# Optimization experiments

Measured on AMD Instinct MI355X. Metric: run time of the kernel, lower is better.

The kernel has to match this reference:

```python
import jax, jax.numpy as jnp
import numpy as np

C = 1.0
MIN_NORM = 1e-15
BALL_EPS = 4e-3  # hgcn eps for float32 in proj

def _norm(v):
    return jnp.maximum(jnp.linalg.norm(v, axis=-1, keepdims=True), MIN_NORM)

def artanh(y):
    return jnp.arctanh(jnp.clip(y, -1.0 + 1e-7, 1.0 - 1e-7))

def logmap0(p, c):
    sqrt_c = c ** 0.5
    pn = _norm(p)
    return p / (sqrt_c * pn) * artanh(sqrt_c * pn)

def expmap0(u, c):
    sqrt_c = c ** 0.5
    un = _norm(u)
    return jnp.tanh(sqrt_c * un) * u / (sqrt_c * un)

def proj(x, c):
    xn = _norm(x)
    maxnorm = (1.0 - BALL_EPS) / (c ** 0.5)
    return jnp.where(xn > maxnorm, x / xn * maxnorm, x)

def setup_inputs() -> dict:
    key = jax.random.key(0)
    k1, k2, k3, k4 = jax.random.split(key, 4)
    N, E, F = 100000, 640000, 128
    # points inside the Poincare ball
    x = 0.01 * jax.random.normal(k1, (N, F), dtype=jnp.float32)
    adj = jax.random.randint(k2, (2, E), 0, N, dtype=jnp.int64)
    edge_attr = jax.random.normal(k3, (E, F), dtype=jnp.float32)
    att_w = jax.random.normal(k4, (1, 3 * F), dtype=jnp.float32) * (1.0 / np.sqrt(3 * F))
    att_b = jnp.zeros((1,), dtype=jnp.float32)
    return {"x": x, "adj": adj, "edge_attr": edge_attr, "att_w": att_w, "att_b": att_b}

def reference(x, adj, edge_attr, att_w, att_b):
    N = x.shape[0]
    src, dst = adj[0], adj[1]  # agg_direction='in' -> i = 0
    xt = logmap0(x, C)  # [N, F] tangent features
    xs = xt[src]        # [E, F] gathered neighbor tangent feats
    # DenseAtt: sigmoid(Linear(cat(x_i, x_j, edge_attr)))
    feats = jnp.concatenate([xs, xt[dst], edge_attr], axis=-1)  # [E, 3F]
    adj_att = jax.nn.sigmoid(feats @ att_w.T + att_b)           # [E, 1]
    ones = jnp.ones((src.shape[0], 1), dtype=xt.dtype)
    agg_add = jax.ops.segment_sum(xs * adj_att, src, num_segments=N)
    cnt_src = jnp.maximum(jax.ops.segment_sum(ones, src, num_segments=N), 1.0)
    cnt_dst = jnp.maximum(jax.ops.segment_sum(ones, dst, num_segments=N), 1.0)
    mean_src = jax.ops.segment_sum(edge_attr, src, num_segments=N) / cnt_src
    mean_dst = jax.ops.segment_sum(edge_attr, dst, num_segments=N) / cnt_dst
    support_t = xt + agg_add + mean_src + mean_dst
    return proj(expmap0(support_t, C), C)
```

## Files before the change

### kernel.cpp

```cpp
#include <hip/hip_runtime.h>
#include <math.h>

#define F 128
#define WAVE 64
#define CAP 64
#define LSLOT 32

__global__ void k_zero(int* __restrict__ p, int n) {
    int i = blockIdx.x * blockDim.x + threadIdx.x;
    if (i < n) p[i] = 0;
}

__device__ __forceinline__ float halfwave_reduce_sum(float v) {
#pragma unroll
    for (int off = 16; off >= 1; off >>= 1)
        v += __shfl_xor(v, off, 64);
    return v;
}

__global__ void k_prenode(const float* __restrict__ x, const float* __restrict__ w,
                          float* __restrict__ a_s, float* __restrict__ a_d, int N) {
    int row = blockIdx.x * (blockDim.x >> 5) + (threadIdx.x >> 5);
    int fl = threadIdx.x & 31;
    if (row >= N) return;
    float4 v = ((const float4*)(x + (size_t)row * F))[fl];
    float ss = halfwave_reduce_sum(v.x * v.x + v.y * v.y + v.z * v.z + v.w * v.w);
    float pn = fmaxf(sqrtf(ss), 1e-15f);
    float y = fminf(pn, 1.0f - 1e-7f);
    float at = 0.5f * __logf((1.0f + y) / (1.0f - y));
    float s = at / pn;
    float4 o = make_float4(v.x * s, v.y * s, v.z * s, v.w * s);
    float4 W0 = ((const float4*)w)[fl];
    float4 W1 = ((const float4*)(w + F))[fl];
    float d0 = halfwave_reduce_sum(o.x * W0.x + o.y * W0.y + o.z * W0.z + o.w * W0.w);
    float d1 = halfwave_reduce_sum(o.x * W1.x + o.y * W1.y + o.z * W1.z + o.w * W1.w);
    if (fl == 0) { a_s[row] = d0; a_d[row] = d1; }
}

__global__ void k_fill(const int* __restrict__ src, const int* __restrict__ dst,
                       const float* __restrict__ a_d,
                       int* __restrict__ cur_src, int* __restrict__ cur_dst,
                       int* __restrict__ elist_src, int* __restrict__ elist_dst,
                       float* __restrict__ ad_e, int E) {
    int e = blockIdx.x * blockDim.x + threadIdx.x;
    if (e >= E) return;
    int s = src[e], d = dst[e];
    ad_e[e] = a_d[d];
    int ps = atomicAdd(&cur_src[s], 1);
    if (ps < CAP) elist_src[(size_t)s * CAP + ps] = e;
    int pd = atomicAdd(&cur_dst[d], 1);
    if (pd < CAP) elist_dst[(size_t)d * CAP + pd] = e;
}

__global__ __launch_bounds__(128) void
k_aggfinal(const float* __restrict__ x, const float* __restrict__ eattr,
           const int* __restrict__ cur_src, const int* __restrict__ cur_dst,
           const int* __restrict__ elist_src, const int* __restrict__ elist_dst,
           const float* __restrict__ a_s, const float* __restrict__ ad_e,
           const float* __restrict__ w, const float* __restrict__ bptr,
           float* __restrict__ out, int N) {
    __shared__ float dot_lds[2][LSLOT * 33];
    int wid  = threadIdx.x >> 6;
    int lane = threadIdx.x & (WAVE - 1);
    int n = blockIdx.x * 2 + wid;
    if (n >= N) return;
    float* dlds = dot_lds[wid];
    int half = lane >> 5;
    int fl   = lane & 31;

    int cS = cur_src[n]; int degS = cS < CAP ? cS : CAP;
    int cD = cur_dst[n]; int degD = cD < CAP ? cD : CAP;
    int e_lnS = (lane < degS) ? elist_src[(size_t)n * CAP + lane] : 0;
    int e_lnD = (lane < degD) ? elist_dst[(size_t)n * CAP + lane] : 0;
    float advl = (lane < degS) ? ad_e[e_lnS] : 0.f;

    float4 W2 = ((const float4*)(w + 2 * F))[fl];
    float a_sn = a_s[n];
    float bias = bptr[0];

    float4 accS0 = make_float4(0.f, 0.f, 0.f, 0.f), accS1 = accS0;
    float4 accD0 = accS0, accD1 = accS0;
    float attsum_fb = 0.f;
    int degM = degS > degD ? degS : degD;
    for (int i = 0; i < degM; i += 4) {
        int idx0 = i + half;
        int idx1 = i + 2 + half;
        int eS0 = __shfl(e_lnS, idx0, 64);
        int eS1 = __shfl(e_lnS, idx1, 64);
        int eD0 = __shfl(e_lnD, idx0, 64);
        int eD1 = __shfl(e_lnD, idx1, 64);
        if (idx0 < degD) {
            float4 v = ((const float4*)(eattr + (size_t)eD0 * F))[fl];
            accD0.x += v.x; accD0.y += v.y; accD0.z += v.z; accD0.w += v.w;
        }
        if (idx1 < degD) {
            float4 v = ((const float4*)(eattr + (size_t)eD1 * F))[fl];
            accD1.x += v.x; accD1.y += v.y; accD1.z += v.z; accD1.w += v.w;
        }
        if (idx0 < degS) {
            float4 v = ((const float4*)(eattr + (size_t)eS0 * F))[fl];
            accS0.x += v.x; accS0.y += v.y; accS0.z += v.z; accS0.w += v.w;
            float p = v.x * W2.x + v.y * W2.y + v.z * W2.z + v.w * W2.w;
            if (idx0 < LSLOT) {
                dlds[idx0 * 33 + fl] = p;
            } else {
                float adv = __shfl(advl, idx0, 64);
                float dotv = halfwave_reduce_sum(p);
                attsum_fb += 1.0f / (1.0f + __expf(-(a_sn + adv + dotv + bias)));
            }
        }
        if (idx1 < degS) {
            float4 v = ((const float4*)(eattr + (size_t)eS1 * F))[fl];
            accS1.x += v.x; accS1.y += v.y; accS1.z += v.z; accS1.w += v.w;
            float p = v.x * W2.x + v.y * W2.y + v.z * W2.z + v.w * W2.w;
            if (idx1 < LSLOT) {
                dlds[idx1 * 33 + fl] = p;
            } else {
                float adv = __shfl(advl, idx1, 64);
                float dotv = halfwave_reduce_sum(p);
                attsum_fb += 1.0f / (1.0f + __expf(-(a_sn + adv + dotv + bias)));
            }
        }
    }
    float4 accS = make_float4(accS0.x + accS1.x, accS0.y + accS1.y,
                              accS0.z + accS1.z, accS0.w + accS1.w);
    float4 accD = make_float4(accD0.x + accD1.x, accD0.y + accD1.y,
                              accD0.z + accD1.z, accD0.w + accD1.w);
    accS.x += __shfl_xor(accS.x, 32, 64); accS.y += __shfl_xor(accS.y, 32, 64);
    accS.z += __shfl_xor(accS.z, 32, 64); accS.w += __shfl_xor(accS.w, 32, 64);
    accD.x += __shfl_xor(accD.x, 32, 64); accD.y += __shfl_xor(accD.y, 32, 64);
    accD.z += __shfl_xor(accD.z, 32, 64); accD.w += __shfl_xor(accD.w, 32, 64);
    attsum_fb += __shfl_xor(attsum_fb, 32, 64);

    int mS = degS < LSLOT ? degS : LSLOT;
    float att_l = 0.f;
    if (lane < mS) {
        float d0 = 0.f, d1 = 0.f, d2 = 0.f, d3 = 0.f;
#pragma unroll
        for (int k = 0; k < 32; k += 4) {
            d0 += dlds[lane * 33 + k];
            d1 += dlds[lane * 33 + k + 1];
            d2 += dlds[lane * 33 + k + 2];
            d3 += dlds[lane * 33 + k + 3];
        }
        float dotv = (d0 + d1) + (d2 + d3);
        att_l = 1.0f / (1.0f + __expf(-(a_sn + advl + dotv + bias)));
    }
    float attsum = att_l;
#pragma unroll
    for (int off = 32; off >= 1; off >>= 1)
        attsum += __shfl_xor(attsum, off, 64);
    attsum += attsum_fb;

    float4 xv = ((const float4*)(x + (size_t)n * F))[fl];
    float ssx = halfwave_reduce_sum(xv.x * xv.x + xv.y * xv.y + xv.z * xv.z + xv.w * xv.w);
    float pnx = fmaxf(sqrtf(ssx), 1e-15f);
    float yx = fminf(pnx, 1.0f - 1e-7f);
    float atx = 0.5f * __logf((1.0f + yx) / (1.0f - yx));
    float sx = atx / pnx;

    float invS = 1.0f / fmaxf((float)cS, 1.0f);
    float invD = 1.0f / fmaxf((float)cD, 1.0f);
    float fa = (1.0f + attsum) * sx;
    float4 u;
    u.x = xv.x * fa + accS.x * invS + accD.x * invD;
    u.y = xv.y * fa + accS.y * invS + accD.y * invD;
    u.z = xv.z * fa + accS.z * invS + accD.z * invD;
    u.w = xv.w * fa + accS.w * invS + accD.w * invD;

    float pp = halfwave_reduce_sum(u.x * u.x + u.y * u.y + u.z * u.z + u.w * u.w);
    float un = fmaxf(sqrtf(pp), 1e-15f);
    float ex = __expf(2.0f * un);
    float t = 1.0f - 2.0f / (ex + 1.0f);
    float scale = fminf(t, 1.0f - 4e-3f) / un;
    if (half == 0) {
        float4 o = make_float4(u.x * scale, u.y * scale, u.z * scale, u.w * scale);
        ((float4*)(out + (size_t)n * F))[fl] = o;
    }
}

extern "C" void kernel_launch(void* const* d_in, const int* in_sizes, int n_in,
                              void* d_out, int out_size, void* d_ws, size_t ws_size,
                              hipStream_t stream) {
    const float* x      = (const float*)d_in[0];
    const int*   adj    = (const int*)d_in[1];
    const float* eattr  = (const float*)d_in[2];
    const float* att_w  = (const float*)d_in[3];
    const float* att_b  = (const float*)d_in[4];
    float* out = (float*)d_out;

    const int N = in_sizes[0] / F;
    const int E = in_sizes[1] / 2;
    const int* src = adj;
    const int* dst = adj + E;

    char* ws = (char*)d_ws;
    size_t off = 0;
    float* a_s       = (float*)(ws + off); off += (size_t)N * sizeof(float);
    float* a_d       = (float*)(ws + off); off += (size_t)N * sizeof(float);
    float* ad_e      = (float*)(ws + off); off += (size_t)E * sizeof(float);
    int*   elist_src = (int*)  (ws + off); off += (size_t)N * CAP * sizeof(int);
    int*   elist_dst = (int*)  (ws + off); off += (size_t)N * CAP * sizeof(int);
    int*   zblock    = (int*)  (ws + off);
    int*   cur_src   = zblock;
    int*   cur_dst   = zblock + N;

    dim3 blk(256);
    const int HPB = 256 / 32;

    k_zero    <<<(2 * N + 255) / 256, blk, 0, stream>>>(zblock, 2 * N);
    k_prenode <<<(N + HPB - 1) / HPB, blk, 0, stream>>>(x, att_w, a_s, a_d, N);
    k_fill    <<<(E + 255) / 256, blk, 0, stream>>>(src, dst, a_d, cur_src, cur_dst,
                                                    elist_src, elist_dst, ad_e, E);
    k_aggfinal<<<(N + 1) / 2, dim3(128), 0, stream>>>(x, eattr,
                cur_src, cur_dst, elist_src, elist_dst, a_s, ad_e, att_w, att_b, out, N);
}
```

Before: 259.9 us.

## Merge prenode and fill kernels, drop per-edge ad_e buffer, vectorize zeroing

Combines the node-attention precompute and the edge-list fill into a single launch by splitting the grid into two block ranges. The per-edge ad_e array goes away: the aggregation kernel now looks up dst[e] and reads a_d[dst] itself, adding one dependent gather per edge. Zeroing of the counters uses float4 stores, and the output write becomes a nontemporal store. The goal is to cut one launch and the extra per-edge traffic, at the cost of a longer dependent load chain in the main kernel. The float4 zeroing assumes 2*N is a multiple of 4.

```diff
diff --git a/kernel.cpp b/kernel.cpp
--- a/kernel.cpp
+++ b/kernel.cpp
@@ -6,9 +6,11 @@
 #define CAP 64
 #define LSLOT 32
 
-__global__ void k_zero(int* __restrict__ p, int n) {
+typedef float f4_t __attribute__((ext_vector_type(4)));
+
+__global__ void k_zero(float4* __restrict__ p, int n4) {
     int i = blockIdx.x * blockDim.x + threadIdx.x;
-    if (i < n) p[i] = 0;
+    if (i < n4) p[i] = make_float4(0.f, 0.f, 0.f, 0.f);
 }
 
 __device__ __forceinline__ float halfwave_reduce_sum(float v) {
@@ -18,45 +20,46 @@
     return v;
 }
 
-__global__ void k_prenode(const float* __restrict__ x, const float* __restrict__ w,
-                          float* __restrict__ a_s, float* __restrict__ a_d, int N) {
-    int row = blockIdx.x * (blockDim.x >> 5) + (threadIdx.x >> 5);
-    int fl = threadIdx.x & 31;
-    if (row >= N) return;
-    float4 v = ((const float4*)(x + (size_t)row * F))[fl];
-    float ss = halfwave_reduce_sum(v.x * v.x + v.y * v.y + v.z * v.z + v.w * v.w);
-    float pn = fmaxf(sqrtf(ss), 1e-15f);
-    float y = fminf(pn, 1.0f - 1e-7f);
-    float at = 0.5f * __logf((1.0f + y) / (1.0f - y));
-    float s = at / pn;
-    float4 o = make_float4(v.x * s, v.y * s, v.z * s, v.w * s);
-    float4 W0 = ((const float4*)w)[fl];
-    float4 W1 = ((const float4*)(w + F))[fl];
-    float d0 = halfwave_reduce_sum(o.x * W0.x + o.y * W0.y + o.z * W0.z + o.w * W0.w);
-    float d1 = halfwave_reduce_sum(o.x * W1.x + o.y * W1.y + o.z * W1.z + o.w * W1.w);
-    if (fl == 0) { a_s[row] = d0; a_d[row] = d1; }
-}
-
-__global__ void k_fill(const int* __restrict__ src, const int* __restrict__ dst,
-                       const float* __restrict__ a_d,
-                       int* __restrict__ cur_src, int* __restrict__ cur_dst,
-                       int* __restrict__ elist_src, int* __restrict__ elist_dst,
-                       float* __restrict__ ad_e, int E) {
-    int e = blockIdx.x * blockDim.x + threadIdx.x;
-    if (e >= E) return;
-    int s = src[e], d = dst[e];
-    ad_e[e] = a_d[d];
-    int ps = atomicAdd(&cur_src[s], 1);
-    if (ps < CAP) elist_src[(size_t)s * CAP + ps] = e;
-    int pd = atomicAdd(&cur_dst[d], 1);
-    if (pd < CAP) elist_dst[(size_t)d * CAP + pd] = e;
+__global__ void k_fillpre(const int* __restrict__ src, const int* __restrict__ dst,
+                          const float* __restrict__ x, const float* __restrict__ w,
+                          int* __restrict__ cur_src, int* __restrict__ cur_dst,
+                          int* __restrict__ elist_src, int* __restrict__ elist_dst,
+                          float* __restrict__ a_s, float* __restrict__ a_d,
+                          int B1, int N, int E) {
+    int b = blockIdx.x;
+    if (b < B1) {
+        int e = b * 256 + threadIdx.x;
+        if (e >= E) return;
+        int s = src[e], d = dst[e];
+        int ps = atomicAdd(&cur_src[s], 1);
+        if (ps < CAP) elist_src[(size_t)s * CAP + ps] = e;
+        int pd = atomicAdd(&cur_dst[d], 1);
+        if (pd < CAP) elist_dst[(size_t)d * CAP + pd] = e;
+    } else {
+        int row = (b - B1) * 8 + (threadIdx.x >> 5);
+        int fl = threadIdx.x & 31;
+        if (row >= N) return;
+        float4 v = ((const float4*)(x + (size_t)row * F))[fl];
+        float ss = halfwave_reduce_sum(v.x * v.x + v.y * v.y + v.z * v.z + v.w * v.w);
+        float pn = fmaxf(sqrtf(ss), 1e-15f);
+        float y = fminf(pn, 1.0f - 1e-7f);
+        float at = 0.5f * __logf((1.0f + y) / (1.0f - y));
+        float s = at / pn;
+        float4 o = make_float4(v.x * s, v.y * s, v.z * s, v.w * s);
+        float4 W0 = ((const float4*)w)[fl];
+        float4 W1 = ((const float4*)(w + F))[fl];
+        float d0 = halfwave_reduce_sum(o.x * W0.x + o.y * W0.y + o.z * W0.z + o.w * W0.w);
+        float d1 = halfwave_reduce_sum(o.x * W1.x + o.y * W1.y + o.z * W1.z + o.w * W1.w);
+        if (fl == 0) { a_s[row] = d0; a_d[row] = d1; }
+    }
 }
 
 __global__ __launch_bounds__(128) void
 k_aggfinal(const float* __restrict__ x, const float* __restrict__ eattr,
+           const int* __restrict__ dst,
            const int* __restrict__ cur_src, const int* __restrict__ cur_dst,
            const int* __restrict__ elist_src, const int* __restrict__ elist_dst,
-           const float* __restrict__ a_s, const float* __restrict__ ad_e,
+           const float* __restrict__ a_s, const float* __restrict__ a_d,
            const float* __restrict__ w, const float* __restrict__ bptr,
            float* __restrict__ out, int N) {
     __shared__ float dot_lds[2][LSLOT * 33];
@@ -72,7 +75,8 @@
     int cD = cur_dst[n]; int degD = cD < CAP ? cD : CAP;
     int e_lnS = (lane < degS) ? elist_src[(size_t)n * CAP + lane] : 0;
     int e_lnD = (lane < degD) ? elist_dst[(size_t)n * CAP + lane] : 0;
-    float advl = (lane < degS) ? ad_e[e_lnS] : 0.f;
+    int dstv  = (lane < degS) ? dst[e_lnS] : 0;
+    float advl = (lane < degS) ? a_d[dstv] : 0.f;
 
     float4 W2 = ((const float4*)(w + 2 * F))[fl];
     float a_sn = a_s[n];
@@ -174,8 +178,9 @@
     float t = 1.0f - 2.0f / (ex + 1.0f);
     float scale = fminf(t, 1.0f - 4e-3f) / un;
     if (half == 0) {
-        float4 o = make_float4(u.x * scale, u.y * scale, u.z * scale, u.w * scale);
-        ((float4*)(out + (size_t)n * F))[fl] = o;
+        f4_t o;
+        o.x = u.x * scale; o.y = u.y * scale; o.z = u.z * scale; o.w = u.w * scale;
+        __builtin_nontemporal_store(o, (f4_t*)(out + (size_t)n * F) + fl);
     }
 }
 
@@ -198,7 +203,6 @@
     size_t off = 0;
     float* a_s       = (float*)(ws + off); off += (size_t)N * sizeof(float);
     float* a_d       = (float*)(ws + off); off += (size_t)N * sizeof(float);
-    float* ad_e      = (float*)(ws + off); off += (size_t)E * sizeof(float);
     int*   elist_src = (int*)  (ws + off); off += (size_t)N * CAP * sizeof(int);
     int*   elist_dst = (int*)  (ws + off); off += (size_t)N * CAP * sizeof(int);
     int*   zblock    = (int*)  (ws + off);
@@ -206,12 +210,13 @@
     int*   cur_dst   = zblock + N;
 
     dim3 blk(256);
-    const int HPB = 256 / 32;
-
-    k_zero    <<<(2 * N + 255) / 256, blk, 0, stream>>>(zblock, 2 * N);
-    k_prenode <<<(N + HPB - 1) / HPB, blk, 0, stream>>>(x, att_w, a_s, a_d, N);
-    k_fill    <<<(E + 255) / 256, blk, 0, stream>>>(src, dst, a_d, cur_src, cur_dst,
-                                                    elist_src, elist_dst, ad_e, E);
-    k_aggfinal<<<(N + 1) / 2, dim3(128), 0, stream>>>(x, eattr,
-                cur_src, cur_dst, elist_src, elist_dst, a_s, ad_e, att_w, att_b, out, N);
-}
+    const int n4 = (2 * N) / 4;
+    const int B1 = (E + 255) / 256;
+    const int B2 = (N + 7) / 8;
+
+    k_zero    <<<(n4 + 255) / 256, blk, 0, stream>>>((float4*)zblock, n4);
+    k_fillpre <<<B1 + B2, blk, 0, stream>>>(src, dst, x, att_w, cur_src, cur_dst,
+                elist_src, elist_dst, a_s, a_d, B1, N, E);
+    k_aggfinal<<<(N + 1) / 2, dim3(128), 0, stream>>>(x, eattr, dst,
+                cur_src, cur_dst, elist_src, elist_dst, a_s, a_d, att_w, att_b, out, N);
+}
```

After: 270.1 us. 1.04x slower.
